# Optimization experiments

Hardware: AMD Instinct MI355X
Metric: run time of the kernel (lower is better)

The kernel has to match this reference:

```python
import jax, jax.numpy as jnp
import numpy as np

B, S, HID = 1, 2048, 2048
H, NOPE, ROPE, VDIM = 16, 128, 64, 128
KV_LORA, Q_LORA = 512, 1536
IH, ID = 16, 128          # index_n_heads, index_head_dim
TOPK = 1024               # config.index_topk
EPS = 1e-6
SCALING = ID ** -0.5      # config.index_head_dim ** -0.5


def setup_inputs() -> dict:
    key = jax.random.key(0)
    ks = jax.random.split(key, 12)
    f = lambda k, sh, sc=1.0: jax.random.normal(k, sh, dtype=jnp.float32) * sc
    # rotary tables (interleave variant uses cat(freqs, freqs) layout)
    pos = jnp.arange(S, dtype=jnp.float32)
    inv_freq = 1.0 / (10000.0 ** (jnp.arange(0, ROPE, 2, dtype=jnp.float32) / ROPE))
    emb = jnp.concatenate([pos[:, None] * inv_freq[None, :]] * 2, axis=-1)  # [S, ROPE]
    return {
        "q_latent": f(ks[0], (B, S, Q_LORA)),
        "hidden_states": f(ks[1], (B, S, HID)),
        "cos": jnp.broadcast_to(jnp.cos(emb)[None], (B, S, ROPE)),
        "sin": jnp.broadcast_to(jnp.sin(emb)[None], (B, S, ROPE)),
        "q_pass": f(ks[2], (B, H, S, NOPE)),
        "q_rot": f(ks[3], (B, H, S, ROPE)),
        "k_pass": f(ks[4], (B, S, KV_LORA)),
        "k_rot": f(ks[5], (B, 1, S, ROPE)),
        "position_ids": jnp.broadcast_to(jnp.arange(S, dtype=jnp.int32)[None], (B, S)),
        "kv_b_weight": f(ks[6], (H * (NOPE + VDIM), KV_LORA), 0.02),
        "wq_b_w": f(ks[7], (IH * ID, Q_LORA), 0.02),
        "wk_w": f(ks[8], (ID, HID), 0.02),
        "k_norm_w": jnp.ones((ID - ROPE,), jnp.float32),
        "wproj_w": f(ks[9], (IH, HID), 0.02),
        "wproj_b": jnp.zeros((IH,), jnp.float32),
    }


def _rotate_half(x):
    x1, x2 = jnp.split(x, 2, axis=-1)
    return jnp.concatenate([-x2, x1], axis=-1)


def _deinterleave(x):
    # view(..., d//2, 2).transpose(-1,-2).reshape(..., d)
    d = x.shape[-1]
    return x.reshape(x.shape[:-1] + (d // 2, 2)).swapaxes(-1, -2).reshape(x.shape)


def _apply_rope_interleave(q, k, cos, sin):
    cos, sin = cos[:, None], sin[:, None]  # unsqueeze head dim
    q, k = _deinterleave(q), _deinterleave(k)
    return q * cos + _rotate_half(q) * sin, k * cos + _rotate_half(k) * sin


def _rmsnorm(x, w):
    var = jnp.mean(x * x, axis=-1, keepdims=True)
    return x * jax.lax.rsqrt(var + EPS) * w


def _sparse_attn_one(q, kv, index_q, index_k, w):
    # q [S,H,576], kv [S,576], index_q [S,IH,ID], index_k [S,ID], w [S,IH]
    s = q.shape[0]
    causal = jnp.arange(s)[:, None] >= jnp.arange(s)[None, :]
    # lightning indexer: sum_h w[q,h] * relu(scale * iq . ik)
    idx_logits = jax.nn.relu(jnp.einsum('qhd,kd->qhk', index_q, index_k) * SCALING)
    idx_score = jnp.einsum('qhk,qh->qk', idx_logits, w)
    idx_score = jnp.where(causal, idx_score, -jnp.inf)
    _, top_idx = jax.lax.top_k(idx_score, TOPK)
    sel = jnp.zeros((s, s), bool).at[jnp.arange(s)[:, None], top_idx].set(True)
    mask = sel & causal  # invalid top-k picks (all -inf, k>q) are killed by causal
    logits = jnp.einsum('qhd,kd->qhk', q, kv) * SCALING
    logits = jnp.where(mask[:, None, :], logits, -jnp.inf)
    attn = jax.nn.softmax(logits, axis=-1)
    return jnp.einsum('qhk,kr->qhr', attn, kv[:, :KV_LORA])  # MLA-absorbed value


def reference(q_latent, hidden_states, cos, sin, q_pass, q_rot, k_pass, k_rot,
              position_ids, kv_b_weight, wq_b_w, wk_w, k_norm_w, wproj_w, wproj_b):
    kv_b = kv_b_weight.reshape(H, NOPE + VDIM, KV_LORA)
    k_b, v_b = kv_b[:, :NOPE], kv_b[:, NOPE:]
    q_abs = jnp.einsum('bhsd,hdr->bhsr', q_pass, k_b)              # absorb k_b into q
    q = jnp.concatenate([q_abs, q_rot], -1).transpose(0, 2, 1, 3)   # [B,S,H,576]
    kv = jnp.concatenate([k_pass, k_rot[:, 0]], -1)                 # [B,S,576]
    # indexer Q/K (index_absorb branch, rmsnorm)
    ql = (q_latent @ wq_b_w.T).reshape(B, S, IH, ID).transpose(0, 2, 1, 3)  # [B,IH,S,ID]
    iq_rot, iq_pass = ql[..., :ROPE], ql[..., ROPE:]
    ckv = hidden_states @ wk_w.T                                    # [B,S,ID]
    ik_rot, ik_pass = ckv[..., :ROPE], ckv[..., ROPE:]
    ik_pass = _rmsnorm(ik_pass, k_norm_w)[:, None]                  # [B,1,S,ID-ROPE]
    iq_rot, ik_rot = _apply_rope_interleave(iq_rot, ik_rot[:, None], cos, sin)
    index_q = jnp.concatenate([iq_rot, iq_pass], -1).transpose(0, 2, 1, 3)  # [B,S,IH,ID]
    index_k = jnp.concatenate([ik_rot, ik_pass], -1)[:, 0]          # [B,S,ID]
    w = jnp.abs(hidden_states @ wproj_w.T + wproj_b)                # index_weights=='value'
    attn_out = jax.vmap(_sparse_attn_one)(q, kv, index_q, index_k, w)  # [B,S,H,KV_LORA]
    return jnp.einsum('bshr,hdr->bshd', attn_out, v_b)              # [B,S,H,VDIM]
```

## Files before the change

kernel.cpp:

```cpp
#include <hip/hip_runtime.h>
#include <hip/hip_bf16.h>

#define S_LEN   2048
#define NH      16
#define ROPE_D  64
#define IDIM    128
#define KV_LORA 512
#define CDIM    576
#define TOPK_K  1024
#define SCALING 0.08838834764831845f

typedef __attribute__((ext_vector_type(4))) float f32x4;
typedef __attribute__((ext_vector_type(8))) short s16x8;
typedef __attribute__((ext_vector_type(4))) int   i32x4;
typedef __attribute__((ext_vector_type(8))) unsigned short u16x8;

static __device__ __forceinline__ unsigned short bf16_bits(float v)
{
    __hip_bfloat16 h = __float2bfloat16(v);
    return *(unsigned short*)&h;
}

#define BM 64
#define BN 64
#define BK 16

#define PKC 256

__global__ __launch_bounds__(256)
void proj_splitk(const float* __restrict__ hidden, const float* __restrict__ wk_w,
                 const float* __restrict__ wproj_w, float* __restrict__ part)
{
    int nt = blockIdx.x, mt = blockIdx.y, ks = blockIdx.z;
    int n0 = nt * 64, m0 = mt * 64, k00 = ks * PKC;
    __shared__ float As[BK][BM + 1];
    __shared__ float Bs[BK][BN + 1];
    int tid = threadIdx.x, tx = tid & 15, ty = tid >> 4;
    float acc[4][4] = {};
    for (int k0 = 0; k0 < PKC; k0 += BK) {
        for (int t = tid; t < BM * BK; t += 256) {
            int m = t >> 4, kk = t & 15;
            As[kk][m] = hidden[(long)(m0 + m) * 2048 + k00 + k0 + kk];
        }
        for (int t = tid; t < BN * BK; t += 256) {
            int nn = t >> 4, kk = t & 15;
            int n = n0 + nn;
            float v = 0.f;
            if (n < 128)      v = wk_w[(long)n * 2048 + k00 + k0 + kk];
            else if (n < 144) v = wproj_w[(long)(n - 128) * 2048 + k00 + k0 + kk];
            Bs[kk][nn] = v;
        }
        __syncthreads();
        #pragma unroll
        for (int kk = 0; kk < BK; kk++) {
            float a[4], b[4];
            #pragma unroll
            for (int i = 0; i < 4; i++) a[i] = As[kk][ty * 4 + i];
            #pragma unroll
            for (int j = 0; j < 4; j++) b[j] = Bs[kk][tx * 4 + j];
            #pragma unroll
            for (int i = 0; i < 4; i++)
                #pragma unroll
                for (int j = 0; j < 4; j++) acc[i][j] += a[i] * b[j];
        }
        __syncthreads();
    }
    for (int i = 0; i < 4; i++) {
        int m = m0 + ty * 4 + i;
        for (int j = 0; j < 4; j++) {
            int n = n0 + tx * 4 + j;
            if (n < 144) part[((long)ks * S_LEN + m) * 144 + n] = acc[i][j];
        }
    }
}

__global__ void proj_reduce(const float* __restrict__ part, float* __restrict__ ckv,
                            float* __restrict__ wmat)
{
    int i = blockIdx.x * 256 + threadIdx.x;
    if (i >= S_LEN * 144) return;
    int m = i / 144, n = i % 144;
    float s = 0.f;
    #pragma unroll
    for (int ks = 0; ks < 8; ks++) s += part[((long)ks * S_LEN + m) * 144 + n];
    if (n < 128) ckv[(long)m * 128 + n] = s;
    else         wmat[(long)m * 16 + (n - 128)] = s;
}

__global__ void pack_split(const float* __restrict__ x, unsigned short* __restrict__ hi,
                           unsigned short* __restrict__ lo, long n)
{
    long i = (long)blockIdx.x * 256 + threadIdx.x;
    if (i < n) {
        float v = x[i];
        __hip_bfloat16 h = __float2bfloat16(v);
        float hv = __bfloat162float(h);
        hi[i] = *(unsigned short*)&h;
        lo[i] = bf16_bits(v - hv);
    }
}

__global__ void pack_bf16(const float* __restrict__ x, unsigned short* __restrict__ y, long n)
{
    long i = (long)blockIdx.x * 256 + threadIdx.x;
    if (i < n) y[i] = bf16_bits(x[i]);
}

__global__ void pack_kbT(const float* __restrict__ kv_b, unsigned short* __restrict__ kbT)
{
    long i = (long)blockIdx.x * 256 + threadIdx.x;
    int k = i & 127, n = (i >> 7) & 511, h = i >> 16;
    kbT[i] = bf16_bits(kv_b[((long)h * 256 + k) * 512 + n]);
}

__global__ void pack_vb(const float* __restrict__ kv_b, unsigned short* __restrict__ vb)
{
    long i = (long)blockIdx.x * 256 + threadIdx.x;
    int r = i & 511, d = (i >> 9) & 127, h = i >> 16;
    vb[i] = bf16_bits(kv_b[((long)h * 256 + 128 + d) * 512 + r]);
}

__global__ void absbias_inplace(float* __restrict__ w, const float* __restrict__ b)
{
    int idx = blockIdx.x * 256 + threadIdx.x;
    if (idx < S_LEN * NH) w[idx] = fabsf(w[idx] + b[idx & 15]);
}

__global__ void rope_iq_inplace(float* __restrict__ ql,
                                const float* __restrict__ cosb,
                                const float* __restrict__ sinb)
{
    int s = blockIdx.x, h = blockIdx.y, i = threadIdx.x;
    float* row = ql + (long)s * (NH * IDIM) + h * IDIM;
    float y  = (i < 32) ? row[2 * i]     : row[2 * (i - 32) + 1];
    float yr = (i < 32) ? -row[2 * i + 1] : row[2 * (i - 32)];
    float c  = cosb[s * ROPE_D + i];
    float sn = sinb[s * ROPE_D + i];
    float val = y * c + yr * sn;
    __syncthreads();
    row[i] = val;
}

__global__ void build_ik_inplace(float* __restrict__ ckv,
                                 const float* __restrict__ cosb,
                                 const float* __restrict__ sinb,
                                 const float* __restrict__ knw)
{
    int k = blockIdx.x, i = threadIdx.x;
    float* row = ckv + (long)k * IDIM;
    float y  = (i < 32) ? row[2 * i]     : row[2 * (i - 32) + 1];
    float yr = (i < 32) ? -row[2 * i + 1] : row[2 * (i - 32)];
    float c  = cosb[k * ROPE_D + i];
    float sn = sinb[k * ROPE_D + i];
    float rot = y * c + yr * sn;
    float xp = row[ROPE_D + i];
    float ss = xp * xp;
    for (int off = 32; off; off >>= 1) ss += __shfl_down(ss, off, 64);
    ss = __shfl(ss, 0, 64);
    float nv = xp * rsqrtf(ss / 64.f + 1e-6f) * knw[i];
    __syncthreads();
    row[i] = rot;
    row[ROPE_D + i] = nv;
}

__global__ __launch_bounds__(256)
void gemm_split3(const unsigned short* __restrict__ Ah, const unsigned short* __restrict__ Al,
                 const unsigned short* __restrict__ Bh, const unsigned short* __restrict__ Bl,
                 float* __restrict__ C, int N, int K, int lda, int ldb, int ldc)
{
    __shared__ __align__(16) unsigned short Bhs[64][136];
    __shared__ __align__(16) unsigned short Bls[64][136];
    int tid = threadIdx.x, wv = tid >> 6, ln = tid & 63, g = ln >> 4, lo = ln & 15;
    int m0 = blockIdx.y * 64 + wv * 16, n0 = blockIdx.x * 64;
    f32x4 acc[4] = {};
    for (int k0 = 0; k0 < K; k0 += 128) {
        __syncthreads();
        for (int i = tid; i < 64 * 16; i += 256) {
            int r = i >> 4, c8 = i & 15;
            *(u16x8*)&Bhs[r][c8 * 8] = *(const u16x8*)&Bh[(long)(n0 + r) * ldb + k0 + c8 * 8];
            *(u16x8*)&Bls[r][c8 * 8] = *(const u16x8*)&Bl[(long)(n0 + r) * ldb + k0 + c8 * 8];
        }
        __syncthreads();
        #pragma unroll
        for (int kc = 0; kc < 128; kc += 32) {
            long aoff = (long)(m0 + lo) * lda + k0 + kc + g * 8;
            s16x8 ah = *(const s16x8*)&Ah[aoff];
            s16x8 al = *(const s16x8*)&Al[aoff];
            #pragma unroll
            for (int nt = 0; nt < 4; nt++) {
                s16x8 bh = *(const s16x8*)&Bhs[nt * 16 + lo][kc + g * 8];
                s16x8 bl = *(const s16x8*)&Bls[nt * 16 + lo][kc + g * 8];
                acc[nt] = __builtin_amdgcn_mfma_f32_16x16x32_bf16(ah, bh, acc[nt], 0, 0, 0);
                acc[nt] = __builtin_amdgcn_mfma_f32_16x16x32_bf16(ah, bl, acc[nt], 0, 0, 0);
                acc[nt] = __builtin_amdgcn_mfma_f32_16x16x32_bf16(al, bh, acc[nt], 0, 0, 0);
            }
        }
    }
    #pragma unroll
    for (int nt = 0; nt < 4; nt++)
        #pragma unroll
        for (int r = 0; r < 4; r++)
            C[(long)(m0 + g * 4 + r) * ldc + n0 + nt * 16 + lo] = acc[nt][r];
}

template<typename TC>
__global__ __launch_bounds__(256)
void gemm_bf16(const unsigned short* __restrict__ A, const unsigned short* __restrict__ B,
               TC* __restrict__ C, int K, int lda, int ldb, int ldc,
               long sA, long sB, long sC)
{
    A += (long)blockIdx.z * sA; B += (long)blockIdx.z * sB; C += (long)blockIdx.z * sC;
    int tid = threadIdx.x, wv = tid >> 6, ln = tid & 63, g = ln >> 4, lo = ln & 15;
    int m0 = blockIdx.y * 64 + wv * 16, n0 = blockIdx.x * 64;
    f32x4 acc[4] = {};
    for (int kc = 0; kc < K; kc += 32) {
        s16x8 a = *(const s16x8*)&A[(long)(m0 + lo) * lda + kc + g * 8];
        #pragma unroll
        for (int nt = 0; nt < 4; nt++) {
            s16x8 b = *(const s16x8*)&B[(long)(n0 + nt * 16 + lo) * ldb + kc + g * 8];
            acc[nt] = __builtin_amdgcn_mfma_f32_16x16x32_bf16(a, b, acc[nt], 0, 0, 0);
        }
    }
    #pragma unroll
    for (int nt = 0; nt < 4; nt++)
        #pragma unroll
        for (int r = 0; r < 4; r++)
            C[(long)(m0 + g * 4 + r) * ldc + n0 + nt * 16 + lo] = (TC)acc[nt][r];
}

__global__ __launch_bounds__(256)
void scores_mfma(const unsigned short* __restrict__ iq_hi, const unsigned short* __restrict__ iq_lo,
                 const unsigned short* __restrict__ ik_hi, const unsigned short* __restrict__ ik_lo,
                 const float* __restrict__ w, float* __restrict__ sc)
{
    int bk = blockIdx.x, bq = blockIdx.y;
    if (bk > bq) return;
    int q0 = bq * 64, k0 = bk * 64;
    __shared__ __align__(16) unsigned short Khi[64][136];
    __shared__ __align__(16) unsigned short Klo[64][136];
    __shared__ float Ws[64][17];
    int tid = threadIdx.x, wv = tid >> 6, ln = tid & 63, g = ln >> 4, lo = ln & 15;

    for (int i = tid; i < 64 * 16; i += 256) {
        int r = i >> 4, c8 = i & 15;
        *(u16x8*)&Khi[r][c8 * 8] = *(const u16x8*)&ik_hi[(long)(k0 + r) * IDIM + c8 * 8];
        *(u16x8*)&Klo[r][c8 * 8] = *(const u16x8*)&ik_lo[(long)(k0 + r) * IDIM + c8 * 8];
    }
    for (int i = tid; i < 64 * 16; i += 256)
        Ws[i >> 4][i & 15] = w[(long)(q0 + (i >> 4)) * NH + (i & 15)];
    __syncthreads();

    float fin[4][4][4] = {};
    #pragma unroll
    for (int hh = 0; hh < 4; hh++) {
        int h = wv * 4 + hh;
        #pragma unroll
        for (int mg = 0; mg < 2; mg++) {
            f32x4 acc[2][4] = {};
            #pragma unroll
            for (int kc = 0; kc < 4; kc++) {
                s16x8 ah[2], al[2];
                #pragma unroll
                for (int mi = 0; mi < 2; mi++) {
                    long off = ((long)(q0 + (mg * 2 + mi) * 16 + lo) * NH + h) * IDIM + kc * 32 + g * 8;
                    ah[mi] = *(const s16x8*)&iq_hi[off];
                    al[mi] = *(const s16x8*)&iq_lo[off];
                }
                #pragma unroll
                for (int nt = 0; nt < 4; nt++) {
                    s16x8 bh = *(const s16x8*)&Khi[nt * 16 + lo][kc * 32 + g * 8];
                    s16x8 bl = *(const s16x8*)&Klo[nt * 16 + lo][kc * 32 + g * 8];
                    #pragma unroll
                    for (int mi = 0; mi < 2; mi++) {
                        acc[mi][nt] = __builtin_amdgcn_mfma_f32_16x16x32_bf16(ah[mi], bh, acc[mi][nt], 0, 0, 0);
                        acc[mi][nt] = __builtin_amdgcn_mfma_f32_16x16x32_bf16(ah[mi], bl, acc[mi][nt], 0, 0, 0);
                        acc[mi][nt] = __builtin_amdgcn_mfma_f32_16x16x32_bf16(al[mi], bh, acc[mi][nt], 0, 0, 0);
                    }
                }
            }
            #pragma unroll
            for (int mi = 0; mi < 2; mi++) {
                int mt = mg * 2 + mi;
                #pragma unroll
                for (int r = 0; r < 4; r++) {
                    float wqh = Ws[mt * 16 + g * 4 + r][h];
                    #pragma unroll
                    for (int nt = 0; nt < 4; nt++) {
                        float v = acc[mi][nt][r] * SCALING;
                        v = v > 0.f ? v : 0.f;
                        fin[mt][nt][r] += v * wqh;
                    }
                }
            }
        }
    }
    __syncthreads();
    float (*FinBuf)[68] = (float(*)[68])&Khi[0][0];
    for (int wt = 0; wt < 4; wt++) {
        if (wv == wt) {
            #pragma unroll
            for (int mt = 0; mt < 4; mt++)
                #pragma unroll
                for (int r = 0; r < 4; r++)
                    #pragma unroll
                    for (int nt = 0; nt < 4; nt++) {
                        if (wt == 0) FinBuf[mt * 16 + g * 4 + r][nt * 16 + lo] = fin[mt][nt][r];
                        else         FinBuf[mt * 16 + g * 4 + r][nt * 16 + lo] += fin[mt][nt][r];
                    }
        }
        __syncthreads();
    }
    for (int i = tid; i < 64 * 16; i += 256) {
        int r = i >> 4, c4 = i & 15;
        *(f32x4*)&sc[(long)(q0 + r) * S_LEN + k0 + c4 * 4] = *(f32x4*)&FinBuf[r][c4 * 4];
    }
}

__device__ __forceinline__ int block_scan_excl(int v, volatile int* lds, int tid, int* total)
{
    lds[tid] = v;
    __syncthreads();
    int x = v;
    for (int off = 1; off < 256; off <<= 1) {
        int y = (tid >= off) ? lds[tid - off] : 0;
        __syncthreads();
        x += y;
        lds[tid] = x;
        __syncthreads();
    }
    int t = lds[255];
    __syncthreads();
    *total = t;
    return x - v;
}

__global__ __launch_bounds__(256)
void topk_kernel(const float* __restrict__ sc, int* __restrict__ sel_idx)
{
    __shared__ int lds[256];
    __shared__ int wsum[4];
    int q = blockIdx.x, tid = threadIdx.x;
    int n = q + 1;
    int* row_sel = sel_idx + (long)q * TOPK_K;
    if (n <= TOPK_K) {
        for (int i = tid; i < n; i += 256) row_sel[i] = i;
        return;
    }
    const float* row = sc + (long)q * S_LEN;
    unsigned bits[8];
    int base = tid * 8;
    #pragma unroll
    for (int i = 0; i < 8; i++) {
        int k = base + i;
        bits[i] = (k < n) ? __float_as_uint(row[k]) : 0u;
    }
    unsigned prefix = 0;
    for (int bit = 30; bit >= 0; bit--) {
        unsigned cand = prefix | (1u << bit);
        int c = 0;
        #pragma unroll
        for (int i = 0; i < 8; i++) c += (bits[i] >= cand) ? 1 : 0;
        for (int off = 32; off; off >>= 1) c += __shfl_down(c, off, 64);
        if ((tid & 63) == 0) wsum[tid >> 6] = c;
        __syncthreads();
        int total = wsum[0] + wsum[1] + wsum[2] + wsum[3];
        __syncthreads();
        if (total >= TOPK_K) prefix = cand;
    }
    unsigned v = prefix;
    int lgt = 0, leq = 0;
    #pragma unroll
    for (int i = 0; i < 8; i++) {
        int k = base + i;
        if (k >= n) break;
        if (bits[i] > v) lgt++;
        else if (bits[i] == v) leq++;
    }
    int tot_gt, tot_eq;
    int gt_off = block_scan_excl(lgt, lds, tid, &tot_gt);
    int eq_off = block_scan_excl(leq, lds, tid, &tot_eq);
    int fill = TOPK_K - tot_gt;
    int gpos = gt_off, epos = eq_off;
    for (int i = 0; i < 8; i++) {
        int k = base + i;
        if (k >= n) break;
        if (bits[i] > v) {
            row_sel[gpos++] = k;
        } else if (bits[i] == v) {
            if (epos < fill) row_sel[tot_gt + epos] = k;
            epos++;
        }
    }
}

__global__ void pack_kv(const float* __restrict__ k_pass, const float* __restrict__ k_rot,
                        __hip_bfloat16* __restrict__ kvb)
{
    int k = blockIdx.x;
    for (int i = threadIdx.x; i < CDIM; i += 256) {
        float v = (i < KV_LORA) ? k_pass[(long)k * KV_LORA + i]
                                : k_rot[(long)k * ROPE_D + (i - KV_LORA)];
        kvb[(long)k * CDIM + i] = __float2bfloat16(v);
    }
}

__global__ void pack_qrot(const float* __restrict__ q_rot, __hip_bfloat16* __restrict__ Qcat)
{
    int q = blockIdx.x;
    for (int j = threadIdx.x; j < NH * ROPE_D; j += 256) {
        int h = j >> 6, i = j & 63;
        Qcat[((long)q * NH + h) * CDIM + KV_LORA + i] =
            __float2bfloat16(q_rot[((long)h * S_LEN + q) * ROPE_D + i]);
    }
}

__global__ __launch_bounds__(256, 2)
void attn_mla9(const __hip_bfloat16* __restrict__ Qcat,
               const __hip_bfloat16* __restrict__ kvb,
               const int* __restrict__ sel_idx,
               unsigned short* __restrict__ Oout)
{
    __shared__ __align__(16) unsigned int Kb[2][9216];
    __shared__ __align__(16) float Sp[4][64][4];

    const int q   = blockIdx.x;
    const int tid = threadIdx.x;
    const int wv  = tid >> 6;
    const int ln  = tid & 63;
    const int g   = ln >> 4, lo = ln & 15;
    const int kh  = wv >> 1, dh = wv & 1;
    const int k_l = ln >> 2, oct = ln & 3;
    const int cnt = (q + 1 < TOPK_K) ? (q + 1) : TOPK_K;
    const int* sel = sel_idx + (long)q * TOPK_K;
    const unsigned short* kvu = (const unsigned short*)kvb;
    const unsigned short* qrow = (const unsigned short*)Qcat + (long)q * NH * CDIM;

    s16x8 Qf[9];
    #pragma unroll
    for (int cc = 0; cc < 9; cc++)
        Qf[cc] = *(const s16x8*)&qrow[lo * CDIM + (dh * 9 + cc) * 32 + g * 8];

    float m_run = -1e30f, l_run = 0.f;
    f32x4 O[8];
    #pragma unroll
    for (int s = 0; s < 8; s++) O[s] = (f32x4){0.f, 0.f, 0.f, 0.f};

    const int ntl = (cnt + 31) >> 5;

    const int wsl16 = (((oct & 1) ^ (k_l >> 3)) << 4);

    f32x4 Vst[9];
    int i0 = ln & 31;
    int selvA = sel[i0 < cnt ? i0 : cnt - 1];
    #pragma unroll
    for (int uu = 0; uu < 9; uu++) {
        int u = wv * 9 + uu, khu = u & 1, cu = u >> 1;
        int row = __shfl(selvA, khu * 16 + k_l, 64);
        Vst[uu] = *(const f32x4*)(kvu + (long)row * CDIM + cu * 32 + oct * 8);
    }
    #pragma unroll
    for (int uu = 0; uu < 9; uu++) {
        int u = wv * 9 + uu, khu = u & 1, cu = u >> 1;
        int byte = (cu * 2 + (oct >> 1)) * 1024 + (khu * 16 + k_l) * 32 + wsl16;
        *(f32x4*)((char*)&Kb[0][0] + byte) = Vst[uu];
    }
    int i1 = 32 + (ln & 31);
    int selvN = sel[i1 < cnt ? i1 : cnt - 1];
    __syncthreads();

    const int sread_key = (kh * 16 + lo) * 32 + ((((g & 1) ^ (lo >> 3)) & 1) << 4);
    const int idxA = (g & 1) * 32 + lo;
    const int idxB = idxA + 16;
    int cur = 0;

    for (int t = 0; t < ntl; t++) {
        const int kb = t * 32;
        const bool hasn = (t + 1 < ntl);

        if (hasn) {
            #pragma unroll
            for (int uu = 0; uu < 9; uu++) {
                int u = wv * 9 + uu, khu = u & 1, cu = u >> 1;
                int row = __shfl(selvN, khu * 16 + k_l, 64);
                Vst[uu] = *(const f32x4*)(kvu + (long)row * CDIM + cu * 32 + oct * 8);
            }
        }
        int ni = kb + 64 + (ln & 31);
        int selvNN = sel[ni < cnt ? ni : cnt - 1];

        const char* Kc = (const char*)&Kb[cur][0];
        f32x4 Sacc = (f32x4){0.f, 0.f, 0.f, 0.f};
        #pragma unroll
        for (int cc = 0; cc < 9; cc++) {
            int c = dh * 9 + cc;
            s16x8 av = *(const s16x8*)(Kc + ((c * 4 + g) >> 1) * 1024 + sread_key);
            Sacc = __builtin_amdgcn_mfma_f32_16x16x32_bf16(av, Qf[cc], Sacc, 0, 0, 0);
        }
        *(f32x4*)&Sp[wv][ln][0] = Sacc;
        __syncthreads();

        f32x4 S0 = *(const f32x4*)&Sp[0][ln][0];
        { f32x4 tmp = *(const f32x4*)&Sp[1][ln][0]; S0 += tmp; }
        f32x4 S1 = *(const f32x4*)&Sp[2][ln][0];
        { f32x4 tmp = *(const f32x4*)&Sp[3][ln][0]; S1 += tmp; }

        float pv[8];
        float mx = -1e30f;
        #pragma unroll
        for (int r = 0; r < 4; r++) {
            float s = S0[r] * SCALING;
            if (kb + g * 4 + r >= cnt) s = -1e30f;
            pv[r] = s;
            mx = fmaxf(mx, s);
        }
        #pragma unroll
        for (int r = 0; r < 4; r++) {
            float s = S1[r] * SCALING;
            if (kb + 16 + g * 4 + r >= cnt) s = -1e30f;
            pv[4 + r] = s;
            mx = fmaxf(mx, s);
        }
        mx = fmaxf(mx, __shfl_xor(mx, 16, 64));
        mx = fmaxf(mx, __shfl_xor(mx, 32, 64));
        float mn = fmaxf(m_run, mx);
        float al = __expf(m_run - mn);
        float sum = 0.f;
        #pragma unroll
        for (int j = 0; j < 8; j++) { float e = __expf(pv[j] - mn); pv[j] = e; sum += e; }
        sum += __shfl_xor(sum, 16, 64);
        sum += __shfl_xor(sum, 32, 64);
        m_run = mn;
        l_run = l_run * al + sum;

        int W00 = (int)((unsigned)bf16_bits(pv[0]) | ((unsigned)bf16_bits(pv[1]) << 16));
        int W01 = (int)((unsigned)bf16_bits(pv[2]) | ((unsigned)bf16_bits(pv[3]) << 16));
        int W10 = (int)((unsigned)bf16_bits(pv[4]) | ((unsigned)bf16_bits(pv[5]) << 16));
        int W11 = (int)((unsigned)bf16_bits(pv[6]) | ((unsigned)bf16_bits(pv[7]) << 16));
        int A0 = __shfl(W00, idxA, 64), A1 = __shfl(W01, idxA, 64);
        int A2 = __shfl(W00, idxB, 64), A3 = __shfl(W01, idxB, 64);
        int B0 = __shfl(W10, idxA, 64), B1 = __shfl(W11, idxA, 64);
        int B2 = __shfl(W10, idxB, 64), B3 = __shfl(W11, idxB, 64);
        i32x4 paw;
        paw[0] = (g < 2) ? A0 : B0;
        paw[1] = (g < 2) ? A1 : B1;
        paw[2] = (g < 2) ? A2 : B2;
        paw[3] = (g < 2) ? A3 : B3;
        s16x8 pa = __builtin_bit_cast(s16x8, paw);

        float alh[4];
        #pragma unroll
        for (int r = 0; r < 4; r++) alh[r] = __shfl(al, g * 4 + r, 64);
        #pragma unroll
        for (int s = 0; s < 8; s++) {
            O[s][0] *= alh[0]; O[s][1] *= alh[1]; O[s][2] *= alh[2]; O[s][3] *= alh[3];
        }

        const char* Kpv = Kc + wv * 8192 + g * 256 +
                          ((((lo >> 3) ^ (g & 1)) & 1) << 4) + (lo & 7) * 2;
        #pragma unroll
        for (int s = 0; s < 8; s++) {
            const char* bs = Kpv + s * 1024;
            s16x8 bv;
            #pragma unroll
            for (int j = 0; j < 8; j++)
                bv[j] = *(const short*)(bs + j * 32);
            O[s] = __builtin_amdgcn_mfma_f32_16x16x32_bf16(pa, bv, O[s], 0, 0, 0);
        }

        if (hasn) {
            char* Kn = (char*)&Kb[cur ^ 1][0];
            #pragma unroll
            for (int uu = 0; uu < 9; uu++) {
                int u = wv * 9 + uu, khu = u & 1, cu = u >> 1;
                int byte = (cu * 2 + (oct >> 1)) * 1024 + (khu * 16 + k_l) * 32 + wsl16;
                *(f32x4*)(Kn + byte) = Vst[uu];
            }
        }
        __syncthreads();
        cur ^= 1;
        selvN = selvNN;
    }

    float linv[4];
    #pragma unroll
    for (int r = 0; r < 4; r++) linv[r] = 1.f / __shfl(l_run, g * 4 + r, 64);
    unsigned short* orow = Oout + (long)q * NH * CDIM;
    #pragma unroll
    for (int s = 0; s < 8; s++)
        #pragma unroll
        for (int r = 0; r < 4; r++)
            orow[(g * 4 + r) * KV_LORA + wv * 128 + s * 16 + lo] = bf16_bits(O[s][r] * linv[r]);
}

extern "C" void kernel_launch(void* const* d_in, const int* in_sizes, int n_in,
                              void* d_out, int out_size, void* d_ws, size_t ws_size,
                              hipStream_t stream)
{
    const float* q_latent = (const float*)d_in[0];
    const float* hidden   = (const float*)d_in[1];
    const float* cosp     = (const float*)d_in[2];
    const float* sinp     = (const float*)d_in[3];
    const float* q_pass   = (const float*)d_in[4];
    const float* q_rot    = (const float*)d_in[5];
    const float* k_pass   = (const float*)d_in[6];
    const float* k_rot    = (const float*)d_in[7];
    const float* kv_b     = (const float*)d_in[9];
    const float* wq_b_w   = (const float*)d_in[10];
    const float* wk_w     = (const float*)d_in[11];
    const float* k_norm_w = (const float*)d_in[12];
    const float* wproj_w  = (const float*)d_in[13];
    const float* wproj_b  = (const float*)d_in[14];

    float* ws = (float*)d_ws;
    int* sel_idx = (int*)ws;
    unsigned short* qlat_hi = (unsigned short*)(ws + 2097152);
    unsigned short* qlat_lo = (unsigned short*)(ws + 3670016);
    unsigned short* wq_hi   = (unsigned short*)(ws + 5242880);
    unsigned short* wq_lo   = (unsigned short*)(ws + 6815744);
    float* ql = ws + 8388608;
    unsigned short* iq_hi = (unsigned short*)(ws + 2097152);
    unsigned short* iq_lo = (unsigned short*)(ws + 4194304);
    unsigned short* ik_hi = (unsigned short*)(ws + 6291456);
    unsigned short* ik_lo = (unsigned short*)(ws + 6422528);
    float* wmat = ws + 6553600;
    float* ckv  = ws + 6586368;
    float* sc   = ws + 8388608;
    float* part = ws + 12582912;
    __hip_bfloat16* Qcat = (__hip_bfloat16*)(ws + 2097152);
    __hip_bfloat16* kvb  = (__hip_bfloat16*)(ws + 11534336);
    unsigned short* kbT  = (unsigned short*)(ws + 12124160);
    unsigned short* vb   = (unsigned short*)(ws + 12648448);
    unsigned short* qp   = (unsigned short*)(ws + 13172736);

    dim3 b256(256);
    pack_split<<<dim3(12288), b256, 0, stream>>>(q_latent, qlat_hi, qlat_lo, 2048L * 1536);
    pack_split<<<dim3(12288), b256, 0, stream>>>(wq_b_w, wq_hi, wq_lo, 2048L * 1536);
    gemm_split3<<<dim3(32, 32), b256, 0, stream>>>(qlat_hi, qlat_lo, wq_hi, wq_lo,
        ql, 2048, 1536, 1536, 1536, 2048);
    rope_iq_inplace<<<dim3(2048, 16), dim3(64), 0, stream>>>(ql, cosp, sinp);
    pack_split<<<dim3(16384), b256, 0, stream>>>(ql, iq_hi, iq_lo, 2048L * 2048);
    proj_splitk<<<dim3(3, 32, 8), b256, 0, stream>>>(hidden, wk_w, wproj_w, part);
    proj_reduce<<<dim3((S_LEN * 144 + 255) / 256), b256, 0, stream>>>(part, ckv, wmat);
    build_ik_inplace<<<dim3(2048), dim3(64), 0, stream>>>(ckv, cosp, sinp, k_norm_w);
    pack_split<<<dim3(1024), b256, 0, stream>>>(ckv, ik_hi, ik_lo, 2048L * 128);
    absbias_inplace<<<dim3(128), b256, 0, stream>>>(wmat, wproj_b);
    scores_mfma<<<dim3(32, 32), b256, 0, stream>>>(iq_hi, iq_lo, ik_hi, ik_lo, wmat, sc);
    topk_kernel<<<dim3(2048), b256, 0, stream>>>(sc, sel_idx);

    pack_bf16<<<dim3(16384), b256, 0, stream>>>(q_pass, qp, 16L * 2048 * 128);
    pack_kbT<<<dim3(4096), b256, 0, stream>>>(kv_b, kbT);
    pack_vb<<<dim3(4096), b256, 0, stream>>>(kv_b, vb);
    pack_kv<<<dim3(2048), b256, 0, stream>>>(k_pass, k_rot, kvb);
    gemm_bf16<__hip_bfloat16><<<dim3(8, 32, 16), b256, 0, stream>>>(
        qp, kbT, (__hip_bfloat16*)Qcat, 128, 128, 128, NH * CDIM,
        2048L * 128, 512L * 128, (long)CDIM);
    pack_qrot<<<dim3(2048), b256, 0, stream>>>(q_rot, Qcat);

    attn_mla9<<<dim3(2048), dim3(256), 0, stream>>>(Qcat, kvb, sel_idx,
                                                    (unsigned short*)Qcat);
    gemm_bf16<float><<<dim3(2, 32, 16), b256, 0, stream>>>(
        (const unsigned short*)Qcat, vb, (float*)d_out,
        512, NH * CDIM, KV_LORA, NH * IDIM,
        512L, 128L * 512, (long)IDIM);
}
```

Measured before the change: 785.3 us.

## Transpose V tiles via one-hot MFMA instead of strided LDS short loads

In the sparse MLA attention kernel, the PV step previously assembled each B operand from eight scalar 2-byte LDS reads and built the P operand through eight cross-lane shuffles. The new code reads V rows with 16-byte vector LDS loads and transposes them in registers by multiplying against constant one-hot selector matrices with extra MFMA instructions. It then converts the results back to bf16, which also lets P be packed directly without shuffles. The LDS swizzle is dropped, which may reintroduce bank conflicts. The trade is fewer LDS instructions and shuffles for four extra MFMAs plus conversions per chunk.

```diff
diff --git a/kernel.cpp b/kernel.cpp
--- a/kernel.cpp
+++ b/kernel.cpp
@@ -415,10 +415,10 @@
 }
 
 __global__ __launch_bounds__(256, 2)
-void attn_mla9(const __hip_bfloat16* __restrict__ Qcat,
-               const __hip_bfloat16* __restrict__ kvb,
-               const int* __restrict__ sel_idx,
-               unsigned short* __restrict__ Oout)
+void attn_mla10(const __hip_bfloat16* __restrict__ Qcat,
+                const __hip_bfloat16* __restrict__ kvb,
+                const int* __restrict__ sel_idx,
+                unsigned short* __restrict__ Oout)
 {
     __shared__ __align__(16) unsigned int Kb[2][9216];
     __shared__ __align__(16) float Sp[4][64][4];
@@ -440,6 +440,21 @@
     for (int cc = 0; cc < 9; cc++)
         Qf[cc] = *(const s16x8*)&qrow[lo * CDIM + (dh * 9 + cc) * 32 + g * 8];
 
+    s16x8 sel0v, sel1v;
+    {
+        unsigned onehot = (lo & 1) ? 0x3F800000u : 0x00003F80u;
+        int w = (lo & 7) >> 1;
+        i32x4 s0 = {0, 0, 0, 0}, s1 = {0, 0, 0, 0};
+        #pragma unroll
+        for (int ww = 0; ww < 4; ww++) {
+            s0[ww] = (g == (lo >> 3)     && w == ww) ? (int)onehot : 0;
+            s1[ww] = (g == 2 + (lo >> 3) && w == ww) ? (int)onehot : 0;
+        }
+        sel0v = __builtin_bit_cast(s16x8, s0);
+        sel1v = __builtin_bit_cast(s16x8, s1);
+    }
+    const f32x4 fzero = {0.f, 0.f, 0.f, 0.f};
+
     float m_run = -1e30f, l_run = 0.f;
     f32x4 O[8];
     #pragma unroll
@@ -447,7 +462,6 @@
 
     const int ntl = (cnt + 31) >> 5;
 
-    const int wsl16 = (((oct & 1) ^ (k_l >> 3)) << 4);
 
     f32x4 Vst[9];
     int i0 = ln & 31;
@@ -461,16 +475,14 @@
     #pragma unroll
     for (int uu = 0; uu < 9; uu++) {
         int u = wv * 9 + uu, khu = u & 1, cu = u >> 1;
-        int byte = (cu * 2 + (oct >> 1)) * 1024 + (khu * 16 + k_l) * 32 + wsl16;
+        int byte = (cu * 2 + (oct >> 1)) * 1024 + (khu * 16 + k_l) * 32 + (oct & 1) * 16;
         *(f32x4*)((char*)&Kb[0][0] + byte) = Vst[uu];
     }
     int i1 = 32 + (ln & 31);
     int selvN = sel[i1 < cnt ? i1 : cnt - 1];
     __syncthreads();
 
-    const int sread_key = (kh * 16 + lo) * 32 + ((((g & 1) ^ (lo >> 3)) & 1) << 4);
-    const int idxA = (g & 1) * 32 + lo;
-    const int idxB = idxA + 16;
+    const int sread_key = (kh * 16 + lo) * 32 + ((g & 1) << 4);
     int cur = 0;
 
     for (int t = 0; t < ntl; t++) {
@@ -532,20 +544,9 @@
         m_run = mn;
         l_run = l_run * al + sum;
 
-        int W00 = (int)((unsigned)bf16_bits(pv[0]) | ((unsigned)bf16_bits(pv[1]) << 16));
-        int W01 = (int)((unsigned)bf16_bits(pv[2]) | ((unsigned)bf16_bits(pv[3]) << 16));
-        int W10 = (int)((unsigned)bf16_bits(pv[4]) | ((unsigned)bf16_bits(pv[5]) << 16));
-        int W11 = (int)((unsigned)bf16_bits(pv[6]) | ((unsigned)bf16_bits(pv[7]) << 16));
-        int A0 = __shfl(W00, idxA, 64), A1 = __shfl(W01, idxA, 64);
-        int A2 = __shfl(W00, idxB, 64), A3 = __shfl(W01, idxB, 64);
-        int B0 = __shfl(W10, idxA, 64), B1 = __shfl(W11, idxA, 64);
-        int B2 = __shfl(W10, idxB, 64), B3 = __shfl(W11, idxB, 64);
-        i32x4 paw;
-        paw[0] = (g < 2) ? A0 : B0;
-        paw[1] = (g < 2) ? A1 : B1;
-        paw[2] = (g < 2) ? A2 : B2;
-        paw[3] = (g < 2) ? A3 : B3;
-        s16x8 pa = __builtin_bit_cast(s16x8, paw);
+        s16x8 pa;
+        #pragma unroll
+        for (int e = 0; e < 8; e++) pa[e] = (short)bf16_bits(pv[e]);
 
         float alh[4];
         #pragma unroll
@@ -555,16 +556,26 @@
             O[s][0] *= alh[0]; O[s][1] *= alh[1]; O[s][2] *= alh[2]; O[s][3] *= alh[3];
         }
 
-        const char* Kpv = Kc + wv * 8192 + g * 256 +
-                          ((((lo >> 3) ^ (g & 1)) & 1) << 4) + (lo & 7) * 2;
-        #pragma unroll
-        for (int s = 0; s < 8; s++) {
-            const char* bs = Kpv + s * 1024;
-            s16x8 bv;
-            #pragma unroll
-            for (int j = 0; j < 8; j++)
-                bv[j] = *(const short*)(bs + j * 32);
-            O[s] = __builtin_amdgcn_mfma_f32_16x16x32_bf16(pa, bv, O[s], 0, 0, 0);
+        #pragma unroll
+        for (int cc = 0; cc < 4; cc++) {
+            int c = wv * 4 + cc;
+            const char* abase = Kc + (c * 2 + (g >> 1)) * 1024 + ((g & 1) << 4);
+            s16x8 vt0 = *(const s16x8*)(abase + lo * 32);
+            s16x8 vt1 = *(const s16x8*)(abase + (16 + lo) * 32);
+            f32x4 d00 = __builtin_amdgcn_mfma_f32_16x16x32_bf16(vt0, sel0v, fzero, 0, 0, 0);
+            f32x4 d01 = __builtin_amdgcn_mfma_f32_16x16x32_bf16(vt0, sel1v, fzero, 0, 0, 0);
+            f32x4 d10 = __builtin_amdgcn_mfma_f32_16x16x32_bf16(vt1, sel0v, fzero, 0, 0, 0);
+            f32x4 d11 = __builtin_amdgcn_mfma_f32_16x16x32_bf16(vt1, sel1v, fzero, 0, 0, 0);
+            s16x8 bv0, bv1;
+            #pragma unroll
+            for (int r = 0; r < 4; r++) {
+                bv0[r]     = (short)bf16_bits(d00[r]);
+                bv0[4 + r] = (short)bf16_bits(d10[r]);
+                bv1[r]     = (short)bf16_bits(d01[r]);
+                bv1[4 + r] = (short)bf16_bits(d11[r]);
+            }
+            O[cc * 2]     = __builtin_amdgcn_mfma_f32_16x16x32_bf16(pa, bv0, O[cc * 2], 0, 0, 0);
+            O[cc * 2 + 1] = __builtin_amdgcn_mfma_f32_16x16x32_bf16(pa, bv1, O[cc * 2 + 1], 0, 0, 0);
         }
 
         if (hasn) {
@@ -572,7 +583,7 @@
             #pragma unroll
             for (int uu = 0; uu < 9; uu++) {
                 int u = wv * 9 + uu, khu = u & 1, cu = u >> 1;
-                int byte = (cu * 2 + (oct >> 1)) * 1024 + (khu * 16 + k_l) * 32 + wsl16;
+                int byte = (cu * 2 + (oct >> 1)) * 1024 + (khu * 16 + k_l) * 32 + (oct & 1) * 16;
                 *(f32x4*)(Kn + byte) = Vst[uu];
             }
         }
@@ -656,8 +667,8 @@
         2048L * 128, 512L * 128, (long)CDIM);
     pack_qrot<<<dim3(2048), b256, 0, stream>>>(q_rot, Qcat);
 
-    attn_mla9<<<dim3(2048), dim3(256), 0, stream>>>(Qcat, kvb, sel_idx,
-                                                    (unsigned short*)Qcat);
+    attn_mla10<<<dim3(2048), dim3(256), 0, stream>>>(Qcat, kvb, sel_idx,
+                                                     (unsigned short*)Qcat);
     gemm_bf16<float><<<dim3(2, 32, 16), b256, 0, stream>>>(
         (const unsigned short*)Qcat, vb, (float*)d_out,
         512, NH * CDIM, KV_LORA, NH * IDIM,
```

Result: faster. 739.9 us (-5.8%).
